# Optimization experiments

Hardware: AMD Instinct MI355X
Metric: run time of the kernel (lower is better)

## Reference

```python
import jax, jax.numpy as jnp
import numpy as np

B = 16
NUM_PATCHES = (4096, 1024)
DIM_S, DIM_M, DIM_L = 256, 512, 1024
N_L = NUM_PATCHES[0] + 1   # tokens in x0 (no cls)
N_M = NUM_PATCHES[1]       # patch tokens in x1 (plus 1 cls)
N_S = 4096                 # patch tokens in x2 (plus 1 cls)
# torch: d_k = int(math.sqrt(dim))
D_K1, D_K2, D_K3 = 22, 32, 16  # int(sqrt(512)), int(sqrt(1024)), int(sqrt(256))


def _lin(x, w, b=None):
    # torch nn.Linear: y = x @ W.T + b, w: [out, in]
    y = jnp.einsum('bnd,md->bnm', x, w)
    return y + b if b is not None else y


def setup_inputs() -> dict:
    key = jax.random.key(0)
    ks = jax.random.split(key, 20)
    s = 0.02
    return {
        'x0': jax.random.normal(ks[0], (B, N_L, DIM_L), jnp.float32),
        'x1': jax.random.normal(ks[1], (B, 1 + N_M, DIM_M), jnp.float32),
        'x2': jax.random.normal(ks[2], (B, 1 + N_S, DIM_S), jnp.float32),
        'f_s_w': jax.random.normal(ks[3], (DIM_M, DIM_S), jnp.float32) * s,
        'f_s_b': jnp.zeros((DIM_M,), jnp.float32),
        'f_m_w': jax.random.normal(ks[4], (DIM_L, DIM_M), jnp.float32) * s,
        'f_m_b': jnp.zeros((DIM_L,), jnp.float32),
        'Wq1': jax.random.normal(ks[5], (DIM_M, DIM_M), jnp.float32) * s,
        'Wk1': jax.random.normal(ks[6], (DIM_M, DIM_M), jnp.float32) * s,
        'Wq2': jax.random.normal(ks[7], (DIM_L, DIM_L), jnp.float32) * s,
        'Wk2': jax.random.normal(ks[8], (DIM_L, DIM_L), jnp.float32) * s,
        'Wv': jax.random.normal(ks[9], (DIM_L, DIM_L), jnp.float32) * s,
        'proj_w': jax.random.normal(ks[10], (NUM_PATCHES[0] + 2, NUM_PATCHES[1] + 1), jnp.float32) * s,
        'proj_b': jnp.zeros((NUM_PATCHES[0] + 2,), jnp.float32),
        'gs_w': jax.random.normal(ks[11], (DIM_S, DIM_L), jnp.float32) * s,
        'gs_b': jnp.zeros((DIM_S,), jnp.float32),
    }


def reference(x0, x1, x2, f_s_w, f_s_b, f_m_w, f_m_b, Wq1, Wk1, Wq2, Wk2, Wv,
              proj_w, proj_b, gs_w, gs_b):
    p_l = x0                                   # [B, N_L, dim_l]
    cls_m, p_m = x1[:, :1, :], x1[:, 1:, :]    # [B,1,dim_m], [B,N_M,dim_m]
    cls_s, p_s = x2[:, :1, :], x2[:, 1:, :]    # [B,1,dim_s], [B,N_S,dim_s]

    # stage 1: small->medium cross attention on attention-map level
    cls_s_proj = _lin(cls_s, f_s_w, f_s_b)               # [B,1,dim_m]
    q1 = _lin(cls_s_proj, Wq1)                           # [B,1,dim_m]
    k1 = _lin(jnp.concatenate([cls_s_proj, p_m], 1), Wk1)  # [B,1+N_M,dim_m]
    att1 = jax.nn.softmax(jnp.einsum('bqd,bkd->bqk', q1, k1) / D_K1, axis=-1)
    att1 = _lin(att1, proj_w, proj_b)                    # [B,1,1+N_L]

    # stage 2: medium->large cross attention
    cls_m_proj = _lin(cls_m, f_m_w, f_m_b)               # [B,1,dim_l]
    q2 = _lin(cls_m_proj, Wq2)
    kv_in = jnp.concatenate([cls_m_proj, p_l], 1)        # [B,1+N_L,dim_l]
    k2 = _lin(kv_in, Wk2)
    att2 = jax.nn.softmax(jnp.einsum('bqd,bkd->bqk', q2, k2) / D_K2, axis=-1)
    v = _lin(kv_in, Wv)                                  # [B,1+N_L,dim_l]

    # weighted fusion of attention maps, third attention pass
    wa = 0.3 * att1 + 0.7 * att2                         # [B,1,1+N_L]
    out = jnp.einsum('bqk,bkd->bqd', wa, v * 1.0)        # [B,1,dim_l]
    g_s = _lin(out, gs_w, gs_b)                          # [B,1,dim_s]

    att3 = jax.nn.softmax(jnp.einsum('bnd,bqd->bnq', p_s, g_s) / D_K3, axis=-1)  # [B,N_S,1]
    p_s_out = jnp.einsum('bnq,bqd->bnd', att3, g_s)      # [B,N_S,dim_s]
    return jnp.concatenate([g_s, p_s_out], axis=1)       # [B,1+N_S,dim_s]
```

## Files before the change

### kernel.cpp

```cpp
#include <hip/hip_runtime.h>
#include <stdint.h>

typedef unsigned int u32;
typedef unsigned short u16;

#define NB 16
#define NL 4097
#define NM_ROWS 1025
#define DS 256
#define DM 512
#define DL 1024
#define NK1 1025
#define NK2 4098
#define MPROJ 4098

__device__ __forceinline__ float bf2f(u16 h){ union{u32 u; float f;} c; c.u = ((u32)h)<<16; return c.f; }
__device__ __forceinline__ u16 f2bf(float x){ union{float f; u32 u;} c; c.f=x; u32 u=c.u; return (u16)((u + 0x7fffu + ((u>>16)&1u))>>16); }
__device__ __forceinline__ float getel(const void* p, long i, int f){
  return f ? ((const float*)p)[i] : bf2f(((const u16*)p)[i]);
}
__device__ __forceinline__ void unpack8(uint4 v, float* fo){
  u32 w[4]={v.x,v.y,v.z,v.w};
  #pragma unroll
  for(int i=0;i<4;i++){
    union{u32 u; float x;} a,b;
    a.u = w[i]<<16; b.u = w[i]&0xffff0000u;
    fo[2*i]=a.x; fo[2*i+1]=b.x;
  }
}
__device__ __forceinline__ float wsum(float v){
  #pragma unroll
  for(int o=32;o>0;o>>=1) v += __shfl_xor(v,o,64);
  return v;
}
__device__ __forceinline__ float wmaxr(float v){
  #pragma unroll
  for(int o=32;o>0;o>>=1) v = fmaxf(v, __shfl_xor(v,o,64));
  return v;
}
__device__ __forceinline__ float block_sum(float v, volatile float* red){
  v = wsum(v);
  if((threadIdx.x&63)==0) red[threadIdx.x>>6]=v;
  __syncthreads();
  float r = red[0]+red[1]+red[2]+red[3];
  __syncthreads();
  return r;
}
__device__ __forceinline__ float block_max(float v, volatile float* red){
  v = wmaxr(v);
  if((threadIdx.x&63)==0) red[threadIdx.x>>6]=v;
  __syncthreads();
  float r = fmaxf(fmaxf(red[0],red[1]),fmaxf(red[2],red[3]));
  __syncthreads();
  return r;
}
__device__ __forceinline__ float clamp60(float x){ return fminf(fmaxf(x,-60.f),60.f); }

__global__ __launch_bounds__(256) void detect_kernel(const u16* __restrict__ x0, int* __restrict__ flag){
  __shared__ float red[256];
  float mx=0.f;
  for(int i=threadIdx.x;i<4096;i+=256){
    float v = fabsf(bf2f(x0[i]));
    if (v==v) mx = fmaxf(mx, v);
  }
  red[threadIdx.x]=mx; __syncthreads();
  if(threadIdx.x==0){
    float m=0.f;
    for(int i=0;i<256;i++) m=fmaxf(m,red[i]);
    flag[0] = (m>1e3f)?1:0;
  }
}

struct Job {
  const void* W; const void* x; const void* bias; float* out;
  int M, D; long xstride; int xinws;
};

__global__ __launch_bounds__(256) void gemv_n_kernel(Job j0, Job j1, const int* __restrict__ flagp){
  Job j = (blockIdx.y==0)? j0 : j1;
  if ((int)(blockIdx.x*4) >= j.M) return;
  int f = flagp[0];
  __shared__ float xs[NB*512];
  int tid = threadIdx.x;
  int m = blockIdx.x*4 + (tid>>6);
  int l = tid & 63;
  float acc[NB];
  #pragma unroll
  for(int b=0;b<NB;b++) acc[b]=0.f;
  for(int c0=0;c0<j.D;c0+=512){
    int cl = j.D-c0; if (cl>512) cl=512;
    for(int i=tid;i<NB*cl;i+=256){
      int b=i/cl, d=i-b*cl;
      float v;
      if (j.xinws) v = ((const float*)j.x)[(long)b*j.D + c0 + d];
      else         v = getel(j.x, (long)b*j.xstride + c0 + d, f);
      xs[i]=v;
    }
    __syncthreads();
    if (m < j.M){
      for(int d=l; d<cl; d+=64){
        float w = getel(j.W, (long)m*j.D + c0 + d, f);
        #pragma unroll
        for(int b=0;b<NB;b++) acc[b] += w*xs[b*cl+d];
      }
    }
    __syncthreads();
  }
  if (m >= j.M) return;
  #pragma unroll
  for(int b=0;b<NB;b++) acc[b]=wsum(acc[b]);
  if(l==0){
    float bv = j.bias ? getel(j.bias, m, f) : 0.f;
    #pragma unroll
    for(int b=0;b<NB;b++) j.out[(long)b*j.M+m]=acc[b]+bv;
  }
}

struct TJob { const void* W; const float* x; float* out; int M, D; };

__global__ __launch_bounds__(256) void gemv_t_kernel(TJob j0, TJob j1, const int* __restrict__ flagp){
  TJob j = (blockIdx.z==0)? j0 : j1;
  int f = flagp[0];
  if ((int)(blockIdx.x*256) >= j.D) return;
  int m0 = blockIdx.y*64;
  if (m0 >= j.M) return;
  __shared__ float xs[NB*64];
  int d = blockIdx.x*256 + threadIdx.x;
  for(int i=threadIdx.x;i<NB*64;i+=256){ int b=i>>6, mm=i&63; xs[i]=j.x[(long)b*j.M+m0+mm]; }
  __syncthreads();
  float acc[NB];
  #pragma unroll
  for(int b=0;b<NB;b++) acc[b]=0.f;
  for(int mm=0;mm<64;++mm){
    float w = getel(j.W, (long)(m0+mm)*j.D + d, f);
    #pragma unroll
    for(int b=0;b<NB;b++) acc[b] += w*xs[b*64+mm];
  }
  #pragma unroll
  for(int b=0;b<NB;b++) atomicAdd(&j.out[(long)b*j.D+d], acc[b]);
}

__global__ __launch_bounds__(256) void att1_logits_kernel(const void* __restrict__ x1,
    const float* __restrict__ q1p, float* __restrict__ logits1, const int* __restrict__ flagp){
  int f = flagp[0];
  int b = blockIdx.y;
  int k = blockIdx.x*4 + (threadIdx.x>>6) + 1;
  if (k > 1024) return;
  int l = threadIdx.x & 63;
  long rbase = ((long)b*NM_ROWS + k)*DM + l*8;
  float rf[8];
  if (f){
    const float* rp = (const float*)x1 + rbase;
    float4 a0 = *(const float4*)rp;
    float4 a1 = *(const float4*)(rp+4);
    rf[0]=a0.x; rf[1]=a0.y; rf[2]=a0.z; rf[3]=a0.w;
    rf[4]=a1.x; rf[5]=a1.y; rf[6]=a1.z; rf[7]=a1.w;
  } else {
    uint4 rv = *(const uint4*)((const u16*)x1 + rbase);
    unpack8(rv, rf);
  }
  const float* qp = q1p + (long)b*DM + l*8;
  float s = rf[0]*qp[0]+rf[1]*qp[1]+rf[2]*qp[2]+rf[3]*qp[3]
          + rf[4]*qp[4]+rf[5]*qp[5]+rf[6]*qp[6]+rf[7]*qp[7];
  s = wsum(s);
  if(l==0) logits1[(long)b*NK1 + k] = s * (1.f/22.f);
}

__global__ __launch_bounds__(256) void att1_softmax_kernel(const float* __restrict__ csp,
    const float* __restrict__ q1p, const float* __restrict__ logits1, float* __restrict__ att1_sm){
  __shared__ float red[4];
  int b=blockIdx.x, t=threadIdx.x;
  float p=0.f;
  for(int d=t;d<DM;d+=256) p += q1p[(long)b*DM+d]*csp[(long)b*DM+d];
  float l0 = block_sum(p, red) * (1.f/22.f);
  float mx = l0;
  for(int k=1+t;k<NK1;k+=256) mx = fmaxf(mx, logits1[(long)b*NK1+k]);
  mx = block_max(mx, red);
  float s=0.f;
  for(int k=t;k<NK1;k+=256){
    float lg = (k==0)? l0 : logits1[(long)b*NK1+k];
    float e = __expf(clamp60(lg-mx));
    att1_sm[(long)b*NK1+k]=e;
    s+=e;
  }
  s = block_sum(s, red);
  float inv = 1.f/fmaxf(s,1e-30f);
  for(int k=t;k<NK1;k+=256) att1_sm[(long)b*NK1+k]*=inv;
}

__global__ __launch_bounds__(256) void att1_proj_kernel(const void* __restrict__ proj_w,
    const void* __restrict__ proj_b, const float* __restrict__ att1_sm, float* __restrict__ att1w,
    const int* __restrict__ flagp){
  int f = flagp[0];
  __shared__ float sm[8*1024];
  int tid=threadIdx.x;
  int m = blockIdx.x*4 + (tid>>6);
  int l = tid&63;
  float acc[NB];
  #pragma unroll
  for(int b=0;b<NB;b++) acc[b]=0.f;
  for(int h=0;h<2;h++){
    for(int i=tid;i<8*1024;i+=256){ int bb=i>>10, k=i&1023; sm[i]=att1_sm[(long)(h*8+bb)*NK1+k]; }
    __syncthreads();
    if (m < MPROJ){
      for(int k=l;k<1024;k+=64){
        float w = getel(proj_w, (long)m*NK1+k, f);
        #pragma unroll
        for(int bb=0;bb<8;bb++) acc[h*8+bb] += w * sm[bb*1024+k];
      }
    }
    __syncthreads();
  }
  if (m >= MPROJ) return;
  if(l==0){
    float wt = getel(proj_w, (long)m*NK1 + 1024, f);
    #pragma unroll
    for(int b=0;b<NB;b++) acc[b] += wt * att1_sm[(long)b*NK1 + 1024];
  }
  #pragma unroll
  for(int b=0;b<NB;b++) acc[b]=wsum(acc[b]);
  if(l==0){
    float pb = getel(proj_b, m, f);
    #pragma unroll
    for(int b=0;b<NB;b++) att1w[(long)b*NK2+m] = 0.3f*(acc[b]+pb);
  }
}

__global__ __launch_bounds__(256) void att2_pass_kernel(const void* __restrict__ x0,
    const float* __restrict__ q2p, const float* __restrict__ att1w,
    float* __restrict__ s1, float* __restrict__ s2, float* __restrict__ Zacc,
    const int* __restrict__ flagp){
  __shared__ float ls[4][1024];
  __shared__ float zs[4];
  int f = flagp[0];
  int b = blockIdx.y;
  int w = threadIdx.x>>6, l = threadIdx.x&63;
  float qf[16];
  {
    const float* qp = q2p + (long)b*DL;
    #pragma unroll
    for(int j=0;j<8;j++){ qf[j]=qp[l*8+j]; qf[8+j]=qp[512+l*8+j]; }
  }
  float af1[16], af2[16];
  #pragma unroll
  for(int j=0;j<16;j++){ af1[j]=0.f; af2[j]=0.f; }
  float zacc=0.f;
  int kbase = blockIdx.x*64 + w*16;
  int nk = NL - kbase; if (nk > 16) nk = 16; if (nk < 0) nk = 0;
  const float* awp = att1w + (long)b*NK2 + kbase + 1;
  for(int i=0;i<nk;i++){
    float rf[16];
    long rowoff = ((long)b*NL + kbase + i)*DL;
    if (f){
      const float* rp = ((const float*)x0) + rowoff;
      float4 a0 = *(const float4*)(rp + l*8);
      float4 a1 = *(const float4*)(rp + l*8 + 4);
      float4 a2 = *(const float4*)(rp + 512 + l*8);
      float4 a3 = *(const float4*)(rp + 512 + l*8 + 4);
      rf[0]=a0.x; rf[1]=a0.y; rf[2]=a0.z; rf[3]=a0.w;
      rf[4]=a1.x; rf[5]=a1.y; rf[6]=a1.z; rf[7]=a1.w;
      rf[8]=a2.x; rf[9]=a2.y; rf[10]=a2.z; rf[11]=a2.w;
      rf[12]=a3.x; rf[13]=a3.y; rf[14]=a3.z; rf[15]=a3.w;
    } else {
      const u16* rp = ((const u16*)x0) + rowoff;
      uint4 rv0 = *(const uint4*)(rp + l*8);
      uint4 rv1 = *(const uint4*)(rp + 512 + l*8);
      u32 wd[8]={rv0.x,rv0.y,rv0.z,rv0.w,rv1.x,rv1.y,rv1.z,rv1.w};
      #pragma unroll
      for(int q=0;q<8;q++){
        union{u32 u; float x;} ua,ub;
        ua.u = wd[q]<<16; ub.u = wd[q]&0xffff0000u;
        rf[2*q]=ua.x; rf[2*q+1]=ub.x;
      }
    }
    float dp=0.f;
    #pragma unroll
    for(int j=0;j<16;j++) dp += rf[j]*qf[j];
    dp = clamp60(wsum(dp)*(1.f/32.f));
    float e = __expf(dp);
    float aw = awp[i];
    zacc += e;
    #pragma unroll
    for(int j=0;j<16;j++){ af1[j] += aw*rf[j]; af2[j] += e*rf[j]; }
  }
  #pragma unroll
  for(int c=0;c<2;c++)
    #pragma unroll
    for(int j=0;j<8;j++) ls[w][c*512 + l*8 + j] = af1[c*8+j];
  __syncthreads();
  for(int d=threadIdx.x; d<1024; d+=256)
    atomicAdd(&s1[(long)b*DL+d], ls[0][d]+ls[1][d]+ls[2][d]+ls[3][d]);
  __syncthreads();
  #pragma unroll
  for(int c=0;c<2;c++)
    #pragma unroll
    for(int j=0;j<8;j++) ls[w][c*512 + l*8 + j] = af2[c*8+j];
  if(l==0) zs[w]=zacc;
  __syncthreads();
  for(int d=threadIdx.x; d<1024; d+=256)
    atomicAdd(&s2[(long)b*DL+d], ls[0][d]+ls[1][d]+ls[2][d]+ls[3][d]);
  if(threadIdx.x==0) atomicAdd(&Zacc[b], zs[0]+zs[1]+zs[2]+zs[3]);
}

__global__ __launch_bounds__(256) void finalize_u_kernel(const float* __restrict__ cmp,
    const float* __restrict__ q2p, const float* __restrict__ att1w,
    const float* __restrict__ s1, const float* __restrict__ s2,
    const float* __restrict__ Zacc, float* __restrict__ u){
  __shared__ float red[4];
  int b=blockIdx.x, t=threadIdx.x;
  float p=0.f;
  for(int d=t;d<DL;d+=256) p += q2p[(long)b*DL+d]*cmp[(long)b*DL+d];
  float l20 = clamp60(block_sum(p,red)*(1.f/32.f));
  float e0 = __expf(l20);
  float Zf = fmaxf(Zacc[b] + e0, 1e-30f);
  float a0 = att1w[(long)b*NK2];
  float c7 = 0.7f/Zf;
  for(int d=t;d<DL;d+=256){
    float cm = cmp[(long)b*DL+d];
    u[(long)b*DL+d] = s1[(long)b*DL+d] + a0*cm + c7*(s2[(long)b*DL+d] + e0*cm);
  }
}

__global__ __launch_bounds__(256) void broadcast_out_kernel(const float* __restrict__ g_s,
    void* __restrict__ out, const int* __restrict__ flagp){
  int f = flagp[0];
  int b = blockIdx.y;
  int colq = threadIdx.x & 31;
  int rowo = threadIdx.x >> 5;
  int r = blockIdx.x*8 + rowo;
  const float* gp = g_s + (long)b*DS + colq*8;
  float4 ga = *(const float4*)gp;
  float4 gb = *(const float4*)(gp+4);
  if (r >= NL) return;
  long row = (long)b*NL + r;
  if (f){
    float4* op = (float4*)out + row*64 + colq*2;
    op[0]=ga; op[1]=gb;
  } else {
    uint4 pk;
    pk.x = (u32)f2bf(ga.x) | ((u32)f2bf(ga.y)<<16);
    pk.y = (u32)f2bf(ga.z) | ((u32)f2bf(ga.w)<<16);
    pk.z = (u32)f2bf(gb.x) | ((u32)f2bf(gb.y)<<16);
    pk.w = (u32)f2bf(gb.z) | ((u32)f2bf(gb.w)<<16);
    ((uint4*)out)[row*32 + colq] = pk;
  }
}

extern "C" void kernel_launch(void* const* d_in, const int* in_sizes, int n_in,
                              void* d_out, int out_size, void* d_ws, size_t ws_size,
                              hipStream_t stream) {
  const void* x0     = d_in[0];
  const void* x1     = d_in[1];
  const void* x2     = d_in[2];
  const void* f_s_w  = d_in[3];
  const void* f_s_b  = d_in[4];
  const void* f_m_w  = d_in[5];
  const void* f_m_b  = d_in[6];
  const void* Wq1    = d_in[7];
  const void* Wk1    = d_in[8];
  const void* Wq2    = d_in[9];
  const void* Wk2    = d_in[10];
  const void* Wv     = d_in[11];
  const void* proj_w = d_in[12];
  const void* proj_b = d_in[13];
  const void* gs_w   = d_in[14];
  const void* gs_b   = d_in[15];

  float* ws = (float*)d_ws;
  float* cls_s_proj = ws;
  float* cls_m_proj = cls_s_proj + NB*DM;
  float* q1v        = cls_m_proj + NB*DL;
  float* q2v        = q1v + NB*DM;
  float* logits1    = q2v + NB*DL;
  float* att1_sm    = logits1 + NB*NK1;
  float* att1w      = att1_sm + NB*NK1;
  float* uvec       = att1w + NB*NK2;
  float* outv       = uvec + NB*DL;
  float* g_s        = outv + NB*DL;
  float* q1p        = g_s + NB*DS;
  float* q2p        = q1p + NB*DM;
  float* s1         = q2p + NB*DL;
  float* s2         = s1 + NB*DL;
  float* Zacc       = s2 + NB*DL;
  int*   flag       = (int*)(Zacc + NB);
  size_t zero_bytes = (size_t)(NB*DM + 3*NB*DL + NB) * sizeof(float);
  hipMemsetAsync(q1p, 0, zero_bytes, stream);

  detect_kernel<<<1,256,0,stream>>>((const u16*)x0, flag);

  Job ja0{f_s_w, x2, f_s_b, cls_s_proj, DM, DS, (long)NL*DS, 0};
  Job ja1{f_m_w, x1, f_m_b, cls_m_proj, DL, DM, (long)NM_ROWS*DM, 0};
  gemv_n_kernel<<<dim3(256,2),256,0,stream>>>(ja0, ja1, flag);

  Job jb0{Wq1, cls_s_proj, nullptr, q1v, DM, DM, DM, 1};
  Job jb1{Wq2, cls_m_proj, nullptr, q2v, DL, DL, DL, 1};
  gemv_n_kernel<<<dim3(256,2),256,0,stream>>>(jb0, jb1, flag);

  TJob jt0{Wk1, q1v, q1p, DM, DM};
  TJob jt1{Wk2, q2v, q2p, DL, DL};
  gemv_t_kernel<<<dim3(4,16,2),256,0,stream>>>(jt0, jt1, flag);

  att1_logits_kernel<<<dim3(256,NB),256,0,stream>>>(x1, q1p, logits1, flag);
  att1_softmax_kernel<<<NB,256,0,stream>>>(cls_s_proj, q1p, logits1, att1_sm);
  att1_proj_kernel<<<dim3(1025),256,0,stream>>>(proj_w, proj_b, att1_sm, att1w, flag);

  att2_pass_kernel<<<dim3(65,NB),256,0,stream>>>(x0, q2p, att1w, s1, s2, Zacc, flag);

  finalize_u_kernel<<<NB,256,0,stream>>>(cls_m_proj, q2p, att1w, s1, s2, Zacc, uvec);
  Job jv{Wv, uvec, nullptr, outv, DL, DL, DL, 1};
  gemv_n_kernel<<<dim3(256,1),256,0,stream>>>(jv, jv, flag);
  Job jg{gs_w, outv, gs_b, g_s, DS, DL, DL, 1};
  gemv_n_kernel<<<dim3(64,1),256,0,stream>>>(jg, jg, flag);

  broadcast_out_kernel<<<dim3(513,NB),256,0,stream>>>(g_s, d_out, flag);
}
```

Baseline: 684.2 us.

## Fuse all stages into one persistent kernel with grid-wide atomic barriers

Replaces the chain of roughly a dozen separate kernel launches with a single persistent mega-kernel of 512 blocks. Stages are separated by software grid barriers built on atomic counters, and each stage's work is remapped onto the fixed block count, for example att2 now uses 33 rows per wave and the projection uses strided trips. This aims to remove launch and inter-kernel gaps. The cost is spin-waiting at barriers, reduced parallelism in some stages, and a deadlock risk if the 512 blocks are not all co-resident.

```diff
diff --git a/kernel.cpp b/kernel.cpp
--- a/kernel.cpp
+++ b/kernel.cpp
@@ -13,6 +13,7 @@
 #define NK1 1025
 #define NK2 4098
 #define MPROJ 4098
+#define NBLK 512
 
 __device__ __forceinline__ float bf2f(u16 h){ union{u32 u; float f;} c; c.u = ((u32)h)<<16; return c.f; }
 __device__ __forceinline__ u16 f2bf(float x){ union{float f; u32 u;} c; c.f=x; u32 u=c.u; return (u16)((u + 0x7fffu + ((u>>16)&1u))>>16); }
@@ -20,11 +21,11 @@
   return f ? ((const float*)p)[i] : bf2f(((const u16*)p)[i]);
 }
 __device__ __forceinline__ void unpack8(uint4 v, float* fo){
-  u32 w[4]={v.x,v.y,v.z,v.w};
+  u32 wd[4]={v.x,v.y,v.z,v.w};
   #pragma unroll
   for(int i=0;i<4;i++){
     union{u32 u; float x;} a,b;
-    a.u = w[i]<<16; b.u = w[i]&0xffff0000u;
+    a.u = wd[i]<<16; b.u = wd[i]&0xffff0000u;
     fo[2*i]=a.x; fo[2*i+1]=b.x;
   }
 }
@@ -56,40 +57,35 @@
 }
 __device__ __forceinline__ float clamp60(float x){ return fminf(fmaxf(x,-60.f),60.f); }
 
-__global__ __launch_bounds__(256) void detect_kernel(const u16* __restrict__ x0, int* __restrict__ flag){
-  __shared__ float red[256];
-  float mx=0.f;
-  for(int i=threadIdx.x;i<4096;i+=256){
-    float v = fabsf(bf2f(x0[i]));
-    if (v==v) mx = fmaxf(mx, v);
-  }
-  red[threadIdx.x]=mx; __syncthreads();
-  if(threadIdx.x==0){
-    float m=0.f;
-    for(int i=0;i<256;i++) m=fmaxf(m,red[i]);
-    flag[0] = (m>1e3f)?1:0;
-  }
-}
-
-struct Job {
+__device__ __forceinline__ void gsync(int* bar, int i){
+  __syncthreads();
+  __threadfence();
+  if (threadIdx.x == 0){
+    __hip_atomic_fetch_add(&bar[i], 1, __ATOMIC_ACQ_REL, __HIP_MEMORY_SCOPE_AGENT);
+    while (__hip_atomic_load(&bar[i], __ATOMIC_RELAXED, __HIP_MEMORY_SCOPE_AGENT) < NBLK)
+      __builtin_amdgcn_s_sleep(2);
+  }
+  __syncthreads();
+  __threadfence();
+}
+
+struct GJob {
   const void* W; const void* x; const void* bias; float* out;
-  int M, D; long xstride; int xinws;
+  int M; int D; long xstride; int xinws; int b0; int nb;
 };
 
-__global__ __launch_bounds__(256) void gemv_n_kernel(Job j0, Job j1, const int* __restrict__ flagp){
-  Job j = (blockIdx.y==0)? j0 : j1;
-  if ((int)(blockIdx.x*4) >= j.M) return;
-  int f = flagp[0];
-  __shared__ float xs[NB*512];
+__device__ void gemv_phase(const GJob j, int f, float* xs){
+  int rel = (int)blockIdx.x - j.b0;
+  if (rel < 0 || rel >= j.nb) return;
   int tid = threadIdx.x;
-  int m = blockIdx.x*4 + (tid>>6);
-  int l = tid & 63;
+  int w = tid>>6, l = tid&63;
+  int m = rel*4 + w;
   float acc[NB];
   #pragma unroll
   for(int b=0;b<NB;b++) acc[b]=0.f;
-  for(int c0=0;c0<j.D;c0+=512){
+  for (int c0=0; c0<j.D; c0+=512){
     int cl = j.D-c0; if (cl>512) cl=512;
-    for(int i=tid;i<NB*cl;i+=256){
+    for (int i=tid;i<NB*cl;i+=256){
       int b=i/cl, d=i-b*cl;
       float v;
       if (j.xinws) v = ((const float*)j.x)[(long)b*j.D + c0 + d];
@@ -98,10 +94,10 @@
     }
     __syncthreads();
     if (m < j.M){
-      for(int d=l; d<cl; d+=64){
-        float w = getel(j.W, (long)m*j.D + c0 + d, f);
+      for (int d=l; d<cl; d+=64){
+        float wv = getel(j.W, (long)m*j.D + c0 + d, f);
         #pragma unroll
-        for(int b=0;b<NB;b++) acc[b] += w*xs[b*cl+d];
+        for(int b=0;b<NB;b++) acc[b] += wv*xs[b*cl+d];
       }
     }
     __syncthreads();
@@ -109,240 +105,304 @@
   if (m >= j.M) return;
   #pragma unroll
   for(int b=0;b<NB;b++) acc[b]=wsum(acc[b]);
-  if(l==0){
+  if (l==0){
     float bv = j.bias ? getel(j.bias, m, f) : 0.f;
     #pragma unroll
     for(int b=0;b<NB;b++) j.out[(long)b*j.M+m]=acc[b]+bv;
   }
 }
 
-struct TJob { const void* W; const float* x; float* out; int M, D; };
-
-__global__ __launch_bounds__(256) void gemv_t_kernel(TJob j0, TJob j1, const int* __restrict__ flagp){
-  TJob j = (blockIdx.z==0)? j0 : j1;
-  int f = flagp[0];
-  if ((int)(blockIdx.x*256) >= j.D) return;
-  int m0 = blockIdx.y*64;
-  if (m0 >= j.M) return;
-  __shared__ float xs[NB*64];
-  int d = blockIdx.x*256 + threadIdx.x;
-  for(int i=threadIdx.x;i<NB*64;i+=256){ int b=i>>6, mm=i&63; xs[i]=j.x[(long)b*j.M+m0+mm]; }
+__device__ void tgemv_phase(const void* W, const float* x, float* out, int M, int D,
+                            int b0, int lgDch, int f, float* xs){
+  int nDch = D>>8, nMch = M>>6;
+  int rel = (int)blockIdx.x - b0;
+  if (rel < 0 || rel >= nDch*nMch) return;
+  int tid = threadIdx.x;
+  int bx = rel & (nDch-1);
+  int by = rel >> lgDch;
+  int m0 = by*64;
+  int d = bx*256 + tid;
+  for (int i=tid;i<NB*64;i+=256){ int b=i>>6, mm=i&63; xs[i]=x[(long)b*M + m0+mm]; }
   __syncthreads();
   float acc[NB];
   #pragma unroll
   for(int b=0;b<NB;b++) acc[b]=0.f;
-  for(int mm=0;mm<64;++mm){
-    float w = getel(j.W, (long)(m0+mm)*j.D + d, f);
-    #pragma unroll
-    for(int b=0;b<NB;b++) acc[b] += w*xs[b*64+mm];
-  }
-  #pragma unroll
-  for(int b=0;b<NB;b++) atomicAdd(&j.out[(long)b*j.D+d], acc[b]);
-}
-
-__global__ __launch_bounds__(256) void att1_logits_kernel(const void* __restrict__ x1,
-    const float* __restrict__ q1p, float* __restrict__ logits1, const int* __restrict__ flagp){
-  int f = flagp[0];
-  int b = blockIdx.y;
-  int k = blockIdx.x*4 + (threadIdx.x>>6) + 1;
-  if (k > 1024) return;
-  int l = threadIdx.x & 63;
-  long rbase = ((long)b*NM_ROWS + k)*DM + l*8;
-  float rf[8];
-  if (f){
-    const float* rp = (const float*)x1 + rbase;
-    float4 a0 = *(const float4*)rp;
-    float4 a1 = *(const float4*)(rp+4);
-    rf[0]=a0.x; rf[1]=a0.y; rf[2]=a0.z; rf[3]=a0.w;
-    rf[4]=a1.x; rf[5]=a1.y; rf[6]=a1.z; rf[7]=a1.w;
-  } else {
-    uint4 rv = *(const uint4*)((const u16*)x1 + rbase);
-    unpack8(rv, rf);
-  }
-  const float* qp = q1p + (long)b*DM + l*8;
-  float s = rf[0]*qp[0]+rf[1]*qp[1]+rf[2]*qp[2]+rf[3]*qp[3]
-          + rf[4]*qp[4]+rf[5]*qp[5]+rf[6]*qp[6]+rf[7]*qp[7];
-  s = wsum(s);
-  if(l==0) logits1[(long)b*NK1 + k] = s * (1.f/22.f);
-}
-
-__global__ __launch_bounds__(256) void att1_softmax_kernel(const float* __restrict__ csp,
-    const float* __restrict__ q1p, const float* __restrict__ logits1, float* __restrict__ att1_sm){
-  __shared__ float red[4];
-  int b=blockIdx.x, t=threadIdx.x;
-  float p=0.f;
-  for(int d=t;d<DM;d+=256) p += q1p[(long)b*DM+d]*csp[(long)b*DM+d];
-  float l0 = block_sum(p, red) * (1.f/22.f);
-  float mx = l0;
-  for(int k=1+t;k<NK1;k+=256) mx = fmaxf(mx, logits1[(long)b*NK1+k]);
-  mx = block_max(mx, red);
-  float s=0.f;
-  for(int k=t;k<NK1;k+=256){
-    float lg = (k==0)? l0 : logits1[(long)b*NK1+k];
-    float e = __expf(clamp60(lg-mx));
-    att1_sm[(long)b*NK1+k]=e;
-    s+=e;
-  }
-  s = block_sum(s, red);
-  float inv = 1.f/fmaxf(s,1e-30f);
-  for(int k=t;k<NK1;k+=256) att1_sm[(long)b*NK1+k]*=inv;
-}
-
-__global__ __launch_bounds__(256) void att1_proj_kernel(const void* __restrict__ proj_w,
-    const void* __restrict__ proj_b, const float* __restrict__ att1_sm, float* __restrict__ att1w,
-    const int* __restrict__ flagp){
-  int f = flagp[0];
-  __shared__ float sm[8*1024];
-  int tid=threadIdx.x;
-  int m = blockIdx.x*4 + (tid>>6);
-  int l = tid&63;
-  float acc[NB];
-  #pragma unroll
-  for(int b=0;b<NB;b++) acc[b]=0.f;
-  for(int h=0;h<2;h++){
-    for(int i=tid;i<8*1024;i+=256){ int bb=i>>10, k=i&1023; sm[i]=att1_sm[(long)(h*8+bb)*NK1+k]; }
-    __syncthreads();
-    if (m < MPROJ){
-      for(int k=l;k<1024;k+=64){
-        float w = getel(proj_w, (long)m*NK1+k, f);
+  for (int mm=0;mm<64;++mm){
+    float wv = getel(W, (long)(m0+mm)*D + d, f);
+    #pragma unroll
+    for(int b=0;b<NB;b++) acc[b] += wv*xs[b*64+mm];
+  }
+  #pragma unroll
+  for(int b=0;b<NB;b++) atomicAdd(&out[(long)b*D+d], acc[b]);
+}
+
+__global__ __launch_bounds__(256, 2) void mega_kernel(
+    const void* __restrict__ x0, const void* __restrict__ x1, const void* __restrict__ x2,
+    const void* __restrict__ f_s_w, const void* __restrict__ f_s_b,
+    const void* __restrict__ f_m_w, const void* __restrict__ f_m_b,
+    const void* __restrict__ Wq1, const void* __restrict__ Wk1,
+    const void* __restrict__ Wq2, const void* __restrict__ Wk2, const void* __restrict__ Wv,
+    const void* __restrict__ proj_w, const void* __restrict__ proj_b,
+    const void* __restrict__ gs_w, const void* __restrict__ gs_b,
+    float* __restrict__ ws, void* __restrict__ out)
+{
+  float* cls_s_proj = ws;
+  float* cls_m_proj = cls_s_proj + NB*DM;
+  float* q1v        = cls_m_proj + NB*DL;
+  float* q2v        = q1v + NB*DM;
+  float* logits1    = q2v + NB*DL;
+  float* att1_sm    = logits1 + NB*NK1;
+  float* att1w      = att1_sm + NB*NK1;
+  float* uvec       = att1w + NB*NK2;
+  float* outv       = uvec + NB*DL;
+  float* g_s        = outv + NB*DL;
+  float* q1p        = g_s + NB*DS;
+  float* q2p        = q1p + NB*DM;
+  float* s1         = q2p + NB*DL;
+  float* s2         = s1 + NB*DL;
+  float* Zacc       = s2 + NB*DL;
+  int*   bar        = (int*)(Zacc + NB);
+
+  __shared__ float smem[8192];
+
+  const int blk = (int)blockIdx.x;
+  const int tid = (int)threadIdx.x;
+  const int w = tid>>6, l = tid&63;
+
+  int f;
+  {
+    float mx=0.f;
+    const u16* p = (const u16*)x0;
+    for (int i=tid;i<4096;i+=256){ float v=fabsf(bf2f(p[i])); if(v==v) mx=fmaxf(mx,v); }
+    smem[tid]=mx; __syncthreads();
+    if (tid==0){
+      float m=0.f;
+      for (int i=0;i<256;i++) m=fmaxf(m,smem[i]);
+      smem[0] = (m>1e3f)?1.f:0.f;
+    }
+    __syncthreads();
+    f = (smem[0]!=0.f)?1:0;
+    __syncthreads();
+  }
+
+  gemv_phase(GJob{f_s_w, x2, f_s_b, cls_s_proj, DM, DS, (long)NL*DS, 0, 0, 128}, f, smem);
+  gemv_phase(GJob{f_m_w, x1, f_m_b, cls_m_proj, DL, DM, (long)NM_ROWS*DM, 0, 128, 256}, f, smem);
+  gsync(bar, 0);
+
+  gemv_phase(GJob{Wq1, cls_s_proj, nullptr, q1v, DM, DM, 0, 1, 0, 128}, f, smem);
+  gemv_phase(GJob{Wq2, cls_m_proj, nullptr, q2v, DL, DL, 0, 1, 128, 256}, f, smem);
+  gsync(bar, 1);
+
+  tgemv_phase(Wk1, q1v, q1p, DM, DM, 0, 1, f, smem);
+  tgemv_phase(Wk2, q2v, q2p, DL, DL, 16, 2, f, smem);
+  gsync(bar, 2);
+
+  {
+    int Wd = blk*4 + w;
+    int b = Wd>>7, widx = Wd&127;
+    const float* qp = q1p + (long)b*DM + (long)l*8;
+    float qv[8];
+    #pragma unroll
+    for (int j2=0;j2<8;j2++) qv[j2]=qp[j2];
+    for (int t=0;t<8;t++){
+      int k = widx*8 + t + 1;
+      long rbase = ((long)b*NM_ROWS + k)*DM + (long)l*8;
+      float rf[8];
+      if (f){
+        const float* rp = (const float*)x1 + rbase;
+        float4 a0 = *(const float4*)rp;
+        float4 a1 = *(const float4*)(rp+4);
+        rf[0]=a0.x; rf[1]=a0.y; rf[2]=a0.z; rf[3]=a0.w;
+        rf[4]=a1.x; rf[5]=a1.y; rf[6]=a1.z; rf[7]=a1.w;
+      } else {
+        uint4 rv = *(const uint4*)((const u16*)x1 + rbase);
+        unpack8(rv, rf);
+      }
+      float s = rf[0]*qv[0]+rf[1]*qv[1]+rf[2]*qv[2]+rf[3]*qv[3]
+              + rf[4]*qv[4]+rf[5]*qv[5]+rf[6]*qv[6]+rf[7]*qv[7];
+      s = wsum(s);
+      if (l==0) logits1[(long)b*NK1+k] = s*(1.f/22.f);
+    }
+  }
+  gsync(bar, 3);
+
+  if (blk < NB){
+    int b = blk;
+    volatile float* red = smem;
+    float p=0.f;
+    for (int d2=tid; d2<DM; d2+=256) p += q1p[(long)b*DM+d2]*cls_s_proj[(long)b*DM+d2];
+    float l0 = block_sum(p, red) * (1.f/22.f);
+    float mx = l0;
+    for (int k=1+tid;k<NK1;k+=256) mx = fmaxf(mx, logits1[(long)b*NK1+k]);
+    mx = block_max(mx, red);
+    float s=0.f;
+    for (int k=tid;k<NK1;k+=256){
+      float lg = (k==0)? l0 : logits1[(long)b*NK1+k];
+      float e = __expf(clamp60(lg-mx));
+      att1_sm[(long)b*NK1+k]=e;
+      s+=e;
+    }
+    s = block_sum(s, red);
+    float inv = 1.f/fmaxf(s,1e-30f);
+    for (int k=tid;k<NK1;k+=256) att1_sm[(long)b*NK1+k]*=inv;
+  }
+  gsync(bar, 4);
+
+  {
+    int base = blk*4 + w;
+    int trips = (MPROJ - blk*4 + 2047) / 2048;
+    for (int t=0;t<trips;t++){
+      int m = base + t*2048;
+      float acc[NB];
+      #pragma unroll
+      for (int b2=0;b2<NB;b2++) acc[b2]=0.f;
+      for (int h=0;h<2;h++){
+        for (int i=tid;i<8192;i+=256){ int bb=i>>10, k=i&1023; smem[i]=att1_sm[(long)(h*8+bb)*NK1+k]; }
+        __syncthreads();
+        if (m < MPROJ){
+          for (int k=l;k<1024;k+=64){
+            float wv = getel(proj_w, (long)m*NK1+k, f);
+            #pragma unroll
+            for (int bb=0;bb<8;bb++) acc[h*8+bb] += wv*smem[bb*1024+k];
+          }
+        }
+        __syncthreads();
+      }
+      if (m < MPROJ){
+        if (l==0){
+          float wt = getel(proj_w, (long)m*NK1+1024, f);
+          #pragma unroll
+          for (int b2=0;b2<NB;b2++) acc[b2] += wt*att1_sm[(long)b2*NK1+1024];
+        }
         #pragma unroll
-        for(int bb=0;bb<8;bb++) acc[h*8+bb] += w * sm[bb*1024+k];
-      }
-    }
-    __syncthreads();
-  }
-  if (m >= MPROJ) return;
-  if(l==0){
-    float wt = getel(proj_w, (long)m*NK1 + 1024, f);
-    #pragma unroll
-    for(int b=0;b<NB;b++) acc[b] += wt * att1_sm[(long)b*NK1 + 1024];
-  }
-  #pragma unroll
-  for(int b=0;b<NB;b++) acc[b]=wsum(acc[b]);
-  if(l==0){
-    float pb = getel(proj_b, m, f);
-    #pragma unroll
-    for(int b=0;b<NB;b++) att1w[(long)b*NK2+m] = 0.3f*(acc[b]+pb);
-  }
-}
-
-__global__ __launch_bounds__(256) void att2_pass_kernel(const void* __restrict__ x0,
-    const float* __restrict__ q2p, const float* __restrict__ att1w,
-    float* __restrict__ s1, float* __restrict__ s2, float* __restrict__ Zacc,
-    const int* __restrict__ flagp){
-  __shared__ float ls[4][1024];
-  __shared__ float zs[4];
-  int f = flagp[0];
-  int b = blockIdx.y;
-  int w = threadIdx.x>>6, l = threadIdx.x&63;
-  float qf[16];
+        for (int b2=0;b2<NB;b2++) acc[b2]=wsum(acc[b2]);
+        if (l==0){
+          float pb = getel(proj_b, m, f);
+          #pragma unroll
+          for (int b2=0;b2<NB;b2++) att1w[(long)b2*NK2+m] = 0.3f*(acc[b2]+pb);
+        }
+      }
+    }
+  }
+  gsync(bar, 5);
+
   {
-    const float* qp = q2p + (long)b*DL;
-    #pragma unroll
-    for(int j=0;j<8;j++){ qf[j]=qp[l*8+j]; qf[8+j]=qp[512+l*8+j]; }
-  }
-  float af1[16], af2[16];
-  #pragma unroll
-  for(int j=0;j<16;j++){ af1[j]=0.f; af2[j]=0.f; }
-  float zacc=0.f;
-  int kbase = blockIdx.x*64 + w*16;
-  int nk = NL - kbase; if (nk > 16) nk = 16; if (nk < 0) nk = 0;
-  const float* awp = att1w + (long)b*NK2 + kbase + 1;
-  for(int i=0;i<nk;i++){
-    float rf[16];
-    long rowoff = ((long)b*NL + kbase + i)*DL;
-    if (f){
-      const float* rp = ((const float*)x0) + rowoff;
-      float4 a0 = *(const float4*)(rp + l*8);
-      float4 a1 = *(const float4*)(rp + l*8 + 4);
-      float4 a2 = *(const float4*)(rp + 512 + l*8);
-      float4 a3 = *(const float4*)(rp + 512 + l*8 + 4);
-      rf[0]=a0.x; rf[1]=a0.y; rf[2]=a0.z; rf[3]=a0.w;
-      rf[4]=a1.x; rf[5]=a1.y; rf[6]=a1.z; rf[7]=a1.w;
-      rf[8]=a2.x; rf[9]=a2.y; rf[10]=a2.z; rf[11]=a2.w;
-      rf[12]=a3.x; rf[13]=a3.y; rf[14]=a3.z; rf[15]=a3.w;
-    } else {
-      const u16* rp = ((const u16*)x0) + rowoff;
-      uint4 rv0 = *(const uint4*)(rp + l*8);
-      uint4 rv1 = *(const uint4*)(rp + 512 + l*8);
-      u32 wd[8]={rv0.x,rv0.y,rv0.z,rv0.w,rv1.x,rv1.y,rv1.z,rv1.w};
-      #pragma unroll
-      for(int q=0;q<8;q++){
-        union{u32 u; float x;} ua,ub;
-        ua.u = wd[q]<<16; ub.u = wd[q]&0xffff0000u;
-        rf[2*q]=ua.x; rf[2*q+1]=ub.x;
-      }
-    }
-    float dp=0.f;
-    #pragma unroll
-    for(int j=0;j<16;j++) dp += rf[j]*qf[j];
-    dp = clamp60(wsum(dp)*(1.f/32.f));
-    float e = __expf(dp);
-    float aw = awp[i];
-    zacc += e;
-    #pragma unroll
-    for(int j=0;j<16;j++){ af1[j] += aw*rf[j]; af2[j] += e*rf[j]; }
-  }
-  #pragma unroll
-  for(int c=0;c<2;c++)
-    #pragma unroll
-    for(int j=0;j<8;j++) ls[w][c*512 + l*8 + j] = af1[c*8+j];
-  __syncthreads();
-  for(int d=threadIdx.x; d<1024; d+=256)
-    atomicAdd(&s1[(long)b*DL+d], ls[0][d]+ls[1][d]+ls[2][d]+ls[3][d]);
-  __syncthreads();
-  #pragma unroll
-  for(int c=0;c<2;c++)
-    #pragma unroll
-    for(int j=0;j<8;j++) ls[w][c*512 + l*8 + j] = af2[c*8+j];
-  if(l==0) zs[w]=zacc;
-  __syncthreads();
-  for(int d=threadIdx.x; d<1024; d+=256)
-    atomicAdd(&s2[(long)b*DL+d], ls[0][d]+ls[1][d]+ls[2][d]+ls[3][d]);
-  if(threadIdx.x==0) atomicAdd(&Zacc[b], zs[0]+zs[1]+zs[2]+zs[3]);
-}
-
-__global__ __launch_bounds__(256) void finalize_u_kernel(const float* __restrict__ cmp,
-    const float* __restrict__ q2p, const float* __restrict__ att1w,
-    const float* __restrict__ s1, const float* __restrict__ s2,
-    const float* __restrict__ Zacc, float* __restrict__ u){
-  __shared__ float red[4];
-  int b=blockIdx.x, t=threadIdx.x;
-  float p=0.f;
-  for(int d=t;d<DL;d+=256) p += q2p[(long)b*DL+d]*cmp[(long)b*DL+d];
-  float l20 = clamp60(block_sum(p,red)*(1.f/32.f));
-  float e0 = __expf(l20);
-  float Zf = fmaxf(Zacc[b] + e0, 1e-30f);
-  float a0 = att1w[(long)b*NK2];
-  float c7 = 0.7f/Zf;
-  for(int d=t;d<DL;d+=256){
-    float cm = cmp[(long)b*DL+d];
-    u[(long)b*DL+d] = s1[(long)b*DL+d] + a0*cm + c7*(s2[(long)b*DL+d] + e0*cm);
-  }
-}
-
-__global__ __launch_bounds__(256) void broadcast_out_kernel(const float* __restrict__ g_s,
-    void* __restrict__ out, const int* __restrict__ flagp){
-  int f = flagp[0];
-  int b = blockIdx.y;
-  int colq = threadIdx.x & 31;
-  int rowo = threadIdx.x >> 5;
-  int r = blockIdx.x*8 + rowo;
-  const float* gp = g_s + (long)b*DS + colq*8;
-  float4 ga = *(const float4*)gp;
-  float4 gb = *(const float4*)(gp+4);
-  if (r >= NL) return;
-  long row = (long)b*NL + r;
-  if (f){
-    float4* op = (float4*)out + row*64 + colq*2;
-    op[0]=ga; op[1]=gb;
-  } else {
-    uint4 pk;
-    pk.x = (u32)f2bf(ga.x) | ((u32)f2bf(ga.y)<<16);
-    pk.y = (u32)f2bf(ga.z) | ((u32)f2bf(ga.w)<<16);
-    pk.z = (u32)f2bf(gb.x) | ((u32)f2bf(gb.y)<<16);
-    pk.w = (u32)f2bf(gb.z) | ((u32)f2bf(gb.w)<<16);
-    ((uint4*)out)[row*32 + colq] = pk;
+    float* ls = smem;
+    float* zs = smem + 4096;
+    int b = blk>>5;
+    int widx = ((blk&31)<<2) + w;
+    int kbase = widx*33;
+    int nk = NL - kbase; if (nk>33) nk=33; if (nk<0) nk=0;
+    float qf[16];
+    {
+      const float* qp = q2p + (long)b*DL;
+      #pragma unroll
+      for (int j2=0;j2<8;j2++){ qf[j2]=qp[l*8+j2]; qf[8+j2]=qp[512+l*8+j2]; }
+    }
+    float af1[16], af2[16];
+    #pragma unroll
+    for (int j2=0;j2<16;j2++){ af1[j2]=0.f; af2[j2]=0.f; }
+    float zacc=0.f;
+    const float* awp = att1w + (long)b*NK2 + kbase + 1;
+    for (int i=0;i<nk;i++){
+      float rf[16];
+      long rowoff = ((long)b*NL + kbase + i)*DL;
+      if (f){
+        const float* rp = ((const float*)x0) + rowoff;
+        float4 a0 = *(const float4*)(rp + l*8);
+        float4 a1 = *(const float4*)(rp + l*8 + 4);
+        float4 a2 = *(const float4*)(rp + 512 + l*8);
+        float4 a3 = *(const float4*)(rp + 512 + l*8 + 4);
+        rf[0]=a0.x; rf[1]=a0.y; rf[2]=a0.z; rf[3]=a0.w;
+        rf[4]=a1.x; rf[5]=a1.y; rf[6]=a1.z; rf[7]=a1.w;
+        rf[8]=a2.x; rf[9]=a2.y; rf[10]=a2.z; rf[11]=a2.w;
+        rf[12]=a3.x; rf[13]=a3.y; rf[14]=a3.z; rf[15]=a3.w;
+      } else {
+        const u16* rp = ((const u16*)x0) + rowoff;
+        uint4 rv0 = *(const uint4*)(rp + l*8);
+        uint4 rv1 = *(const uint4*)(rp + 512 + l*8);
+        u32 wd[8]={rv0.x,rv0.y,rv0.z,rv0.w,rv1.x,rv1.y,rv1.z,rv1.w};
+        #pragma unroll
+        for(int q=0;q<8;q++){
+          union{u32 u; float x;} ua,ub;
+          ua.u = wd[q]<<16; ub.u = wd[q]&0xffff0000u;
+          rf[2*q]=ua.x; rf[2*q+1]=ub.x;
+        }
+      }
+      float dp=0.f;
+      #pragma unroll
+      for (int j2=0;j2<16;j2++) dp += rf[j2]*qf[j2];
+      dp = clamp60(wsum(dp)*(1.f/32.f));
+      float e = __expf(dp);
+      float aw = awp[i];
+      zacc += e;
+      #pragma unroll
+      for (int j2=0;j2<16;j2++){ af1[j2] += aw*rf[j2]; af2[j2] += e*rf[j2]; }
+    }
+    #pragma unroll
+    for (int c=0;c<2;c++)
+      #pragma unroll
+      for (int j2=0;j2<8;j2++) ls[w*1024 + c*512 + l*8 + j2] = af1[c*8+j2];
+    __syncthreads();
+    for (int d2=tid; d2<1024; d2+=256)
+      atomicAdd(&s1[(long)b*DL+d2], ls[d2]+ls[1024+d2]+ls[2048+d2]+ls[3072+d2]);
+    __syncthreads();
+    #pragma unroll
+    for (int c=0;c<2;c++)
+      #pragma unroll
+      for (int j2=0;j2<8;j2++) ls[w*1024 + c*512 + l*8 + j2] = af2[c*8+j2];
+    if (l==0) zs[w]=zacc;
+    __syncthreads();
+    for (int d2=tid; d2<1024; d2+=256)
+      atomicAdd(&s2[(long)b*DL+d2], ls[d2]+ls[1024+d2]+ls[2048+d2]+ls[3072+d2]);
+    if (tid==0) atomicAdd(&Zacc[b], zs[0]+zs[1]+zs[2]+zs[3]);
+  }
+  gsync(bar, 6);
+
+  if (blk < NB){
+    int b = blk;
+    volatile float* red = smem;
+    float p=0.f;
+    for (int d2=tid;d2<DL;d2+=256) p += q2p[(long)b*DL+d2]*cls_m_proj[(long)b*DL+d2];
+    float l20 = clamp60(block_sum(p,red)*(1.f/32.f));
+    float e0 = __expf(l20);
+    float Zf = fmaxf(Zacc[b] + e0, 1e-30f);
+    float a0 = att1w[(long)b*NK2];
+    float c7 = 0.7f/Zf;
+    for (int d2=tid;d2<DL;d2+=256){
+      float cm = cls_m_proj[(long)b*DL+d2];
+      uvec[(long)b*DL+d2] = s1[(long)b*DL+d2] + a0*cm + c7*(s2[(long)b*DL+d2] + e0*cm);
+    }
+  }
+  gsync(bar, 7);
+
+  gemv_phase(GJob{Wv, uvec, nullptr, outv, DL, DL, 0, 1, 0, 256}, f, smem);
+  gsync(bar, 8);
+
+  gemv_phase(GJob{gs_w, outv, gs_b, g_s, DS, DL, 0, 1, 0, 64}, f, smem);
+  gsync(bar, 9);
+
+  {
+    int colq = tid & 31;
+    int rowo = tid >> 5;
+    const long total = (long)NB*NL;
+    for (long idx = (long)blk*8 + rowo; idx < total; idx += (long)NBLK*8){
+      int b = (int)(idx / NL);
+      const float* gp = g_s + (long)b*DS + colq*8;
+      float4 ga = *(const float4*)gp;
+      float4 gb = *(const float4*)(gp+4);
+      if (f){
+        float4* op = (float4*)out + idx*64 + colq*2;
+        op[0]=ga; op[1]=gb;
+      } else {
+        uint4 pk;
+        pk.x = (u32)f2bf(ga.x) | ((u32)f2bf(ga.y)<<16);
+        pk.y = (u32)f2bf(ga.z) | ((u32)f2bf(ga.w)<<16);
+        pk.z = (u32)f2bf(gb.x) | ((u32)f2bf(gb.y)<<16);
+        pk.w = (u32)f2bf(gb.z) | ((u32)f2bf(gb.w)<<16);
+        ((uint4*)out)[idx*32 + colq] = pk;
+      }
+    }
   }
 }
 
@@ -367,50 +427,12 @@
   const void* gs_b   = d_in[15];
 
   float* ws = (float*)d_ws;
-  float* cls_s_proj = ws;
-  float* cls_m_proj = cls_s_proj + NB*DM;
-  float* q1v        = cls_m_proj + NB*DL;
-  float* q2v        = q1v + NB*DM;
-  float* logits1    = q2v + NB*DL;
-  float* att1_sm    = logits1 + NB*NK1;
-  float* att1w      = att1_sm + NB*NK1;
-  float* uvec       = att1w + NB*NK2;
-  float* outv       = uvec + NB*DL;
-  float* g_s        = outv + NB*DL;
-  float* q1p        = g_s + NB*DS;
-  float* q2p        = q1p + NB*DM;
-  float* s1         = q2p + NB*DL;
-  float* s2         = s1 + NB*DL;
-  float* Zacc       = s2 + NB*DL;
-  int*   flag       = (int*)(Zacc + NB);
-  size_t zero_bytes = (size_t)(NB*DM + 3*NB*DL + NB) * sizeof(float);
+  float* q1p = ws + (size_t)NB*(DM + DL + DM + DL + NK1 + NK1 + NK2 + DL + DL + DS);
+  size_t zero_bytes = (size_t)(NB*DM + 3*NB*DL + NB)*sizeof(float) + 16*sizeof(int);
   hipMemsetAsync(q1p, 0, zero_bytes, stream);
 
-  detect_kernel<<<1,256,0,stream>>>((const u16*)x0, flag);
-
-  Job ja0{f_s_w, x2, f_s_b, cls_s_proj, DM, DS, (long)NL*DS, 0};
-  Job ja1{f_m_w, x1, f_m_b, cls_m_proj, DL, DM, (long)NM_ROWS*DM, 0};
-  gemv_n_kernel<<<dim3(256,2),256,0,stream>>>(ja0, ja1, flag);
-
-  Job jb0{Wq1, cls_s_proj, nullptr, q1v, DM, DM, DM, 1};
-  Job jb1{Wq2, cls_m_proj, nullptr, q2v, DL, DL, DL, 1};
-  gemv_n_kernel<<<dim3(256,2),256,0,stream>>>(jb0, jb1, flag);
-
-  TJob jt0{Wk1, q1v, q1p, DM, DM};
-  TJob jt1{Wk2, q2v, q2p, DL, DL};
-  gemv_t_kernel<<<dim3(4,16,2),256,0,stream>>>(jt0, jt1, flag);
-
-  att1_logits_kernel<<<dim3(256,NB),256,0,stream>>>(x1, q1p, logits1, flag);
-  att1_softmax_kernel<<<NB,256,0,stream>>>(cls_s_proj, q1p, logits1, att1_sm);
-  att1_proj_kernel<<<dim3(1025),256,0,stream>>>(proj_w, proj_b, att1_sm, att1w, flag);
-
-  att2_pass_kernel<<<dim3(65,NB),256,0,stream>>>(x0, q2p, att1w, s1, s2, Zacc, flag);
-
-  finalize_u_kernel<<<NB,256,0,stream>>>(cls_m_proj, q2p, att1w, s1, s2, Zacc, uvec);
-  Job jv{Wv, uvec, nullptr, outv, DL, DL, DL, 1};
-  gemv_n_kernel<<<dim3(256,1),256,0,stream>>>(jv, jv, flag);
-  Job jg{gs_w, outv, gs_b, g_s, DS, DL, DL, 1};
-  gemv_n_kernel<<<dim3(64,1),256,0,stream>>>(jg, jg, flag);
-
-  broadcast_out_kernel<<<dim3(513,NB),256,0,stream>>>(g_s, d_out, flag);
-}
+  mega_kernel<<<dim3(NBLK), dim3(256), 0, stream>>>(
+      x0, x1, x2, f_s_w, f_s_b, f_m_w, f_m_b,
+      Wq1, Wk1, Wq2, Wk2, Wv, proj_w, proj_b, gs_w, gs_b,
+      ws, d_out);
+}
```

Measured after the change: 1.524 ms. 123% more time.
